# Kernel optimization log

Measured on AMD Instinct MI355X. Metric: run time of the kernel, lower is better.

The kernel has to match this reference:

```python
import jax, jax.numpy as jnp
import numpy as np

EPS_RMS = 1e-6
EPS_Q = 1e-5


def _weight_quant(w):
    # BitNet b1.58-style ternary weight quantization with mean-abs scale
    scale = 1.0 / jnp.clip(jnp.mean(jnp.abs(w)), EPS_Q)
    wq = jnp.clip(jnp.round(w * scale), -1.0, 1.0) / scale
    return w + jax.lax.stop_gradient(wq - w)  # STE


def _activation_quant(x):
    # per-token 8-bit absmax quantization
    scale = 127.0 / jnp.clip(jnp.max(jnp.abs(x), axis=-1, keepdims=True), EPS_Q)
    xq = jnp.clip(jnp.round(x * scale), -128.0, 127.0) / scale
    return x + jax.lax.stop_gradient(xq - x)  # STE


def _rmsnorm(x, weight):
    inv = jax.lax.rsqrt(jnp.mean(x * x, axis=-1, keepdims=True) + EPS_RMS)
    return x * inv * weight


def setup_inputs() -> dict:
    key = jax.random.key(0)
    k1, k2, k3 = jax.random.split(key, 3)
    B, S, D, CD = 8, 4096, 1024, 1024
    x = jax.random.normal(k1, (B, S, D), dtype=jnp.float32)
    c = jax.random.normal(k2, (B, CD), dtype=jnp.float32)
    # NOTE: the module zero-inits proj; we use small random weights so the
    # quantized conditioning path is numerically exercised.
    w_proj = jax.random.normal(k3, (2 * D, CD), dtype=jnp.float32) * 0.02
    b_proj = jnp.zeros((2 * D,), dtype=jnp.float32)
    rms_weight = jnp.ones((D,), dtype=jnp.float32)
    return {"x": x, "c": c, "w_proj": w_proj, "b_proj": b_proj, "rms_weight": rms_weight}


def reference(x, c, w_proj, b_proj, rms_weight):
    if c.ndim == 2:
        c = c[:, None, :]  # [B, 1, cond_dim]
    # BitLinear: quantized activations x quantized ternary weights
    cq = _activation_quant(c)
    wq = _weight_quant(w_proj)
    emb = jnp.einsum('btc,dc->btd', cq, wq) + b_proj  # [B, 1, 2*dim]
    scale, shift = jnp.split(emb, 2, axis=-1)
    xn = _rmsnorm(x, rms_weight)
    return xn * (1.0 + scale) + shift
```

## Files before the change

kernel.cpp:

```cpp
#include <hip/hip_runtime.h>
#include <math.h>


constexpr int Bn = 8;
constexpr int Sn = 4096;
constexpr int Dn = 1024;
constexpr int TWO_D = 2048;
constexpr int OFF_PART = 0;
constexpr int OFF_MW   = 2048;
constexpr int OFF_CQ   = 4096;
constexpr int OFF_SC   = 16384;
constexpr int OFF_SH   = 24576;

__device__ __forceinline__ float waveReduceSum(float v) {
#pragma unroll
    for (int off = 32; off > 0; off >>= 1) v += __shfl_down(v, off, 64);
    return v;
}
__device__ __forceinline__ float waveReduceMax(float v) {
#pragma unroll
    for (int off = 32; off > 0; off >>= 1) v = fmaxf(v, __shfl_down(v, off, 64));
    return v;
}

__global__ void k_absw(const float* __restrict__ w, float* __restrict__ part) {
    int tid = threadIdx.x;
    size_t base = (size_t)blockIdx.x * 1024 + (size_t)tid * 4;
    float4 v = *(const float4*)(w + base);
    float s = fabsf(v.x) + fabsf(v.y) + fabsf(v.z) + fabsf(v.w);
    s = waveReduceSum(s);
    __shared__ float lds[4];
    if ((tid & 63) == 0) lds[tid >> 6] = s;
    __syncthreads();
    if (tid == 0) part[blockIdx.x] = lds[0] + lds[1] + lds[2] + lds[3];
}

__global__ void k_mw(const float* __restrict__ part, float* __restrict__ mw) {
    int tid = threadIdx.x;
    float s = 0.0f;
#pragma unroll
    for (int k = 0; k < 8; ++k) s += part[tid + k * 256];
    s = waveReduceSum(s);
    __shared__ float lds[4];
    if ((tid & 63) == 0) lds[tid >> 6] = s;
    __syncthreads();
    if (tid == 0) {
        float mean = (lds[0] + lds[1] + lds[2] + lds[3]) * (1.0f / 2097152.0f);
        mw[0] = fmaxf(mean, 1e-5f);
    }
}

__global__ void k_cq(const float* __restrict__ c, float* __restrict__ cq) {
    int b = blockIdx.x, tid = threadIdx.x;
    float4 v = ((const float4*)(c + (size_t)b * Dn))[tid];
    float m = fmaxf(fmaxf(fabsf(v.x), fabsf(v.y)), fmaxf(fabsf(v.z), fabsf(v.w)));
    m = waveReduceMax(m);
    __shared__ float lds[4];
    if ((tid & 63) == 0) lds[tid >> 6] = m;
    __syncthreads();
    float mx = fmaxf(fmaxf(lds[0], lds[1]), fmaxf(lds[2], lds[3]));
    float scale = 127.0f / fmaxf(mx, 1e-5f);
    float inv = 1.0f / scale;
    float4 q;
    q.x = fminf(fmaxf(rintf(v.x * scale), -128.0f), 127.0f) * inv;
    q.y = fminf(fmaxf(rintf(v.y * scale), -128.0f), 127.0f) * inv;
    q.z = fminf(fmaxf(rintf(v.z * scale), -128.0f), 127.0f) * inv;
    q.w = fminf(fmaxf(rintf(v.w * scale), -128.0f), 127.0f) * inv;
    ((float4*)(cq + (size_t)b * Dn))[tid] = q;
}

__global__ void k_emb(const float* __restrict__ w, const float* __restrict__ bp,
                      const float* __restrict__ cq, const float* __restrict__ mwp,
                      float* __restrict__ sc, float* __restrict__ sh) {
    int tid = threadIdx.x;
    int lane = tid & 63;
    int d = (blockIdx.x * blockDim.x + tid) >> 6;
    float mw = mwp[0];
    float sw = 1.0f / mw;
    const float* wr = w + (size_t)d * 1024 + (size_t)lane * 16;
    float t[16];
#pragma unroll
    for (int j = 0; j < 16; j += 4) {
        float4 v = *(const float4*)(wr + j);
        t[j + 0] = fminf(fmaxf(rintf(v.x * sw), -1.0f), 1.0f);
        t[j + 1] = fminf(fmaxf(rintf(v.y * sw), -1.0f), 1.0f);
        t[j + 2] = fminf(fmaxf(rintf(v.z * sw), -1.0f), 1.0f);
        t[j + 3] = fminf(fmaxf(rintf(v.w * sw), -1.0f), 1.0f);
    }
    for (int b = 0; b < Bn; ++b) {
        const float* cr = cq + (size_t)b * 1024 + (size_t)lane * 16;
        float dot = 0.0f;
#pragma unroll
        for (int j = 0; j < 16; j += 4) {
            float4 u = *(const float4*)(cr + j);
            dot += t[j + 0] * u.x + t[j + 1] * u.y + t[j + 2] * u.z + t[j + 3] * u.w;
        }
        dot = waveReduceSum(dot);
        if (lane == 0) {
            float val = dot * mw + bp[d];
            if (d < Dn) sc[b * Dn + d] = 1.0f + val;
            else        sh[b * Dn + (d - Dn)] = val;
        }
    }
}

__global__ void k_main(const float* __restrict__ x, const float* __restrict__ rw,
                       const float* __restrict__ sc, const float* __restrict__ sh,
                       float* __restrict__ out) {
    int row = blockIdx.x;
    int b = row >> 12;
    int tid = threadIdx.x;
    float4 v = ((const float4*)(x + (size_t)row * Dn))[tid];
    float ss = v.x * v.x + v.y * v.y + v.z * v.z + v.w * v.w;
    ss = waveReduceSum(ss);
    __shared__ float lds[4];
    if ((tid & 63) == 0) lds[tid >> 6] = ss;
    __syncthreads();
    float tot = lds[0] + lds[1] + lds[2] + lds[3];
    float inv = rsqrtf(tot * (1.0f / 1024.0f) + 1e-6f);
    float4 wv = ((const float4*)rw)[tid];
    float4 s1 = ((const float4*)(sc + (size_t)b * Dn))[tid];
    float4 s0 = ((const float4*)(sh + (size_t)b * Dn))[tid];
    float4 o;
    o.x = v.x * inv * wv.x * s1.x + s0.x;
    o.y = v.y * inv * wv.y * s1.y + s0.y;
    o.z = v.z * inv * wv.z * s1.z + s0.z;
    o.w = v.w * inv * wv.w * s1.w + s0.w;
    ((float4*)(out + (size_t)row * Dn))[tid] = o;
}

extern "C" void kernel_launch(void* const* d_in, const int* in_sizes, int n_in,
                              void* d_out, int out_size, void* d_ws, size_t ws_size,
                              hipStream_t stream) {
    const float* x  = (const float*)d_in[0];
    const float* c  = (const float*)d_in[1];
    const float* w  = (const float*)d_in[2];
    const float* bp = (const float*)d_in[3];
    const float* rw = (const float*)d_in[4];
    float* out = (float*)d_out;
    float* ws  = (float*)d_ws;

    float* part = ws + OFF_PART;
    float* mw   = ws + OFF_MW;
    float* cq   = ws + OFF_CQ;
    float* sc   = ws + OFF_SC;
    float* sh   = ws + OFF_SH;

    k_absw<<<TWO_D, 256, 0, stream>>>(w, part);
    k_mw  <<<1, 256, 0, stream>>>(part, mw);
    k_cq  <<<Bn, 256, 0, stream>>>(c, cq);
    k_emb <<<TWO_D / 4, 256, 0, stream>>>(w, bp, cq, mw, sc, sh);
    k_main<<<Bn * Sn, 256, 0, stream>>>(x, rw, sc, sh, out);
}
```

Measured before the change: 68.58 us.

## Merge prologue kernels and process one row per wavefront in main kernel

Merges the weight abs-sum and activation quantization kernels into one launch, and folds the global mean-abs reduction into every block of the embedding kernel, which drops two kernel launches and their serialization gaps. The main RMSNorm kernel now gives each 64-lane wavefront a full row, so the block-level LDS reduction and barrier are replaced by a single xor-shuffle wave reduction. In exchange, every embedding block redundantly re-reads the 2048 partial sums, and each thread holds four float4 loads in registers.

```diff
diff --git a/kernel.cpp b/kernel.cpp
--- a/kernel.cpp
+++ b/kernel.cpp
@@ -7,76 +7,69 @@
 constexpr int Dn = 1024;
 constexpr int TWO_D = 2048;
 constexpr int OFF_PART = 0;
-constexpr int OFF_MW   = 2048;
 constexpr int OFF_CQ   = 4096;
 constexpr int OFF_SC   = 16384;
 constexpr int OFF_SH   = 24576;
 
-__device__ __forceinline__ float waveReduceSum(float v) {
+__device__ __forceinline__ float waveReduceSumBcast(float v) {
 #pragma unroll
-    for (int off = 32; off > 0; off >>= 1) v += __shfl_down(v, off, 64);
+    for (int off = 32; off > 0; off >>= 1) v += __shfl_xor(v, off, 64);
     return v;
 }
-__device__ __forceinline__ float waveReduceMax(float v) {
+__device__ __forceinline__ float waveReduceMaxBcast(float v) {
 #pragma unroll
-    for (int off = 32; off > 0; off >>= 1) v = fmaxf(v, __shfl_down(v, off, 64));
+    for (int off = 32; off > 0; off >>= 1) v = fmaxf(v, __shfl_xor(v, off, 64));
     return v;
 }
 
-__global__ void k_absw(const float* __restrict__ w, float* __restrict__ part) {
+__global__ void k_pre(const float* __restrict__ w, const float* __restrict__ c,
+                      float* __restrict__ part, float* __restrict__ cq) {
     int tid = threadIdx.x;
-    size_t base = (size_t)blockIdx.x * 1024 + (size_t)tid * 4;
-    float4 v = *(const float4*)(w + base);
-    float s = fabsf(v.x) + fabsf(v.y) + fabsf(v.z) + fabsf(v.w);
-    s = waveReduceSum(s);
-    __shared__ float lds[4];
-    if ((tid & 63) == 0) lds[tid >> 6] = s;
-    __syncthreads();
-    if (tid == 0) part[blockIdx.x] = lds[0] + lds[1] + lds[2] + lds[3];
+    if (blockIdx.x < TWO_D) {
+        size_t base = (size_t)blockIdx.x * 1024 + (size_t)tid * 4;
+        float4 v = *(const float4*)(w + base);
+        float s = fabsf(v.x) + fabsf(v.y) + fabsf(v.z) + fabsf(v.w);
+        s = waveReduceSumBcast(s);
+        __shared__ float lds[4];
+        if ((tid & 63) == 0) lds[tid >> 6] = s;
+        __syncthreads();
+        if (tid == 0) part[blockIdx.x] = lds[0] + lds[1] + lds[2] + lds[3];
+    } else {
+        int b = blockIdx.x - TWO_D;
+        float4 v = ((const float4*)(c + (size_t)b * Dn))[tid];
+        float m = fmaxf(fmaxf(fabsf(v.x), fabsf(v.y)), fmaxf(fabsf(v.z), fabsf(v.w)));
+        m = waveReduceMaxBcast(m);
+        __shared__ float lm[4];
+        if ((tid & 63) == 0) lm[tid >> 6] = m;
+        __syncthreads();
+        float mx = fmaxf(fmaxf(lm[0], lm[1]), fmaxf(lm[2], lm[3]));
+        float scale = 127.0f / fmaxf(mx, 1e-5f);
+        float inv = 1.0f / scale;
+        float4 q;
+        q.x = fminf(fmaxf(rintf(v.x * scale), -128.0f), 127.0f) * inv;
+        q.y = fminf(fmaxf(rintf(v.y * scale), -128.0f), 127.0f) * inv;
+        q.z = fminf(fmaxf(rintf(v.z * scale), -128.0f), 127.0f) * inv;
+        q.w = fminf(fmaxf(rintf(v.w * scale), -128.0f), 127.0f) * inv;
+        ((float4*)(cq + (size_t)b * Dn))[tid] = q;
+    }
 }
 
-__global__ void k_mw(const float* __restrict__ part, float* __restrict__ mw) {
+__global__ void k_emb(const float* __restrict__ w, const float* __restrict__ bp,
+                      const float* __restrict__ cq, const float* __restrict__ part,
+                      float* __restrict__ sc, float* __restrict__ sh) {
     int tid = threadIdx.x;
     float s = 0.0f;
 #pragma unroll
     for (int k = 0; k < 8; ++k) s += part[tid + k * 256];
-    s = waveReduceSum(s);
+    s = waveReduceSumBcast(s);
     __shared__ float lds[4];
     if ((tid & 63) == 0) lds[tid >> 6] = s;
     __syncthreads();
-    if (tid == 0) {
-        float mean = (lds[0] + lds[1] + lds[2] + lds[3]) * (1.0f / 2097152.0f);
-        mw[0] = fmaxf(mean, 1e-5f);
-    }
-}
+    float mw = fmaxf((lds[0] + lds[1] + lds[2] + lds[3]) * (1.0f / 2097152.0f), 1e-5f);
+    float sw = 1.0f / mw;
 
-__global__ void k_cq(const float* __restrict__ c, float* __restrict__ cq) {
-    int b = blockIdx.x, tid = threadIdx.x;
-    float4 v = ((const float4*)(c + (size_t)b * Dn))[tid];
-    float m = fmaxf(fmaxf(fabsf(v.x), fabsf(v.y)), fmaxf(fabsf(v.z), fabsf(v.w)));
-    m = waveReduceMax(m);
-    __shared__ float lds[4];
-    if ((tid & 63) == 0) lds[tid >> 6] = m;
-    __syncthreads();
-    float mx = fmaxf(fmaxf(lds[0], lds[1]), fmaxf(lds[2], lds[3]));
-    float scale = 127.0f / fmaxf(mx, 1e-5f);
-    float inv = 1.0f / scale;
-    float4 q;
-    q.x = fminf(fmaxf(rintf(v.x * scale), -128.0f), 127.0f) * inv;
-    q.y = fminf(fmaxf(rintf(v.y * scale), -128.0f), 127.0f) * inv;
-    q.z = fminf(fmaxf(rintf(v.z * scale), -128.0f), 127.0f) * inv;
-    q.w = fminf(fmaxf(rintf(v.w * scale), -128.0f), 127.0f) * inv;
-    ((float4*)(cq + (size_t)b * Dn))[tid] = q;
-}
-
-__global__ void k_emb(const float* __restrict__ w, const float* __restrict__ bp,
-                      const float* __restrict__ cq, const float* __restrict__ mwp,
-                      float* __restrict__ sc, float* __restrict__ sh) {
-    int tid = threadIdx.x;
     int lane = tid & 63;
     int d = (blockIdx.x * blockDim.x + tid) >> 6;
-    float mw = mwp[0];
-    float sw = 1.0f / mw;
     const float* wr = w + (size_t)d * 1024 + (size_t)lane * 16;
     float t[16];
 #pragma unroll
@@ -95,7 +88,7 @@
             float4 u = *(const float4*)(cr + j);
             dot += t[j + 0] * u.x + t[j + 1] * u.y + t[j + 2] * u.z + t[j + 3] * u.w;
         }
-        dot = waveReduceSum(dot);
+        dot = waveReduceSumBcast(dot);
         if (lane == 0) {
             float val = dot * mw + bp[d];
             if (d < Dn) sc[b * Dn + d] = 1.0f + val;
@@ -104,29 +97,47 @@
     }
 }
 
-__global__ void k_main(const float* __restrict__ x, const float* __restrict__ rw,
-                       const float* __restrict__ sc, const float* __restrict__ sh,
-                       float* __restrict__ out) {
-    int row = blockIdx.x;
-    int b = row >> 12;
-    int tid = threadIdx.x;
-    float4 v = ((const float4*)(x + (size_t)row * Dn))[tid];
-    float ss = v.x * v.x + v.y * v.y + v.z * v.z + v.w * v.w;
-    ss = waveReduceSum(ss);
-    __shared__ float lds[4];
-    if ((tid & 63) == 0) lds[tid >> 6] = ss;
-    __syncthreads();
-    float tot = lds[0] + lds[1] + lds[2] + lds[3];
-    float inv = rsqrtf(tot * (1.0f / 1024.0f) + 1e-6f);
-    float4 wv = ((const float4*)rw)[tid];
-    float4 s1 = ((const float4*)(sc + (size_t)b * Dn))[tid];
-    float4 s0 = ((const float4*)(sh + (size_t)b * Dn))[tid];
-    float4 o;
-    o.x = v.x * inv * wv.x * s1.x + s0.x;
-    o.y = v.y * inv * wv.y * s1.y + s0.y;
-    o.z = v.z * inv * wv.z * s1.z + s0.z;
-    o.w = v.w * inv * wv.w * s1.w + s0.w;
-    ((float4*)(out + (size_t)row * Dn))[tid] = o;
+__global__ void __launch_bounds__(256) k_main(
+        const float* __restrict__ x, const float* __restrict__ rw,
+        const float* __restrict__ sc, const float* __restrict__ sh,
+        float* __restrict__ out) {
+    int tid  = threadIdx.x;
+    int lane = tid & 63;
+    int row  = blockIdx.x * 4 + (tid >> 6);
+    int b    = row >> 12;
+
+    const float4* xr = (const float4*)(x + (size_t)row * Dn);
+    float4 v0 = xr[lane];
+    float4 v1 = xr[lane + 64];
+    float4 v2 = xr[lane + 128];
+    float4 v3 = xr[lane + 192];
+
+    float ss = v0.x*v0.x + v0.y*v0.y + v0.z*v0.z + v0.w*v0.w
+             + v1.x*v1.x + v1.y*v1.y + v1.z*v1.z + v1.w*v1.w
+             + v2.x*v2.x + v2.y*v2.y + v2.z*v2.z + v2.w*v2.w
+             + v3.x*v3.x + v3.y*v3.y + v3.z*v3.z + v3.w*v3.w;
+    ss = waveReduceSumBcast(ss);
+    float inv = rsqrtf(ss * (1.0f / 1024.0f) + 1e-6f);
+
+    const float4* rwv = (const float4*)rw;
+    const float4* s1v = (const float4*)(sc + (size_t)b * Dn);
+    const float4* s0v = (const float4*)(sh + (size_t)b * Dn);
+    float4* ov = (float4*)(out + (size_t)row * Dn);
+
+#pragma unroll
+    for (int q = 0; q < 4; ++q) {
+        int idx = lane + q * 64;
+        float4 v = (q == 0) ? v0 : (q == 1) ? v1 : (q == 2) ? v2 : v3;
+        float4 wv = rwv[idx];
+        float4 s1 = s1v[idx];
+        float4 s0 = s0v[idx];
+        float4 o;
+        o.x = v.x * inv * wv.x * s1.x + s0.x;
+        o.y = v.y * inv * wv.y * s1.y + s0.y;
+        o.z = v.z * inv * wv.z * s1.z + s0.z;
+        o.w = v.w * inv * wv.w * s1.w + s0.w;
+        ov[idx] = o;
+    }
 }
 
 extern "C" void kernel_launch(void* const* d_in, const int* in_sizes, int n_in,
@@ -141,14 +152,11 @@
     float* ws  = (float*)d_ws;
 
     float* part = ws + OFF_PART;
-    float* mw   = ws + OFF_MW;
     float* cq   = ws + OFF_CQ;
     float* sc   = ws + OFF_SC;
     float* sh   = ws + OFF_SH;
 
-    k_absw<<<TWO_D, 256, 0, stream>>>(w, part);
-    k_mw  <<<1, 256, 0, stream>>>(part, mw);
-    k_cq  <<<Bn, 256, 0, stream>>>(c, cq);
-    k_emb <<<TWO_D / 4, 256, 0, stream>>>(w, bp, cq, mw, sc, sh);
-    k_main<<<Bn * Sn, 256, 0, stream>>>(x, rw, sc, sh, out);
+    k_pre <<<TWO_D + Bn, 256, 0, stream>>>(w, c, part, cq);
+    k_emb <<<TWO_D / 4, 256, 0, stream>>>(w, bp, cq, part, sc, sh);
+    k_main<<<Bn * Sn / 4, 256, 0, stream>>>(x, rw, sc, sh, out);
 }
```

Result: faster. 63.30 us (-7.7%).
